# Optimization experiments

Measured on AMD Instinct MI355X. Metric: run time of the kernel, lower is better.

The kernel has to match this reference:

```python
import jax, jax.numpy as jnp
import numpy as np

B, F, D, U = 4096, 32, 64, 256


def setup_inputs() -> dict:
    key = jax.random.key(0)
    k1, k2, k3, k4 = jax.random.split(key, 4)
    embeds = jax.random.normal(k1, (B, F, D), dtype=jnp.float32)
    # glorot-ish scaling for the learned weights
    linear_w = jax.random.normal(k2, (F * D, U), dtype=jnp.float32) * (2.0 / (F * D + U)) ** 0.5
    inner_w = jax.random.normal(k3, (U, F), dtype=jnp.float32) * (2.0 / (U + F)) ** 0.5
    outer_w = jax.random.normal(k4, (U, D, D), dtype=jnp.float32) * (2.0 / (2 * D)) ** 0.5
    return {"embeds": embeds, "linear_w": linear_w, "inner_w": inner_w, "outer_w": outer_w}


def reference(embeds, linear_w, inner_w, outer_w):
    b = embeds.shape[0]
    # linear signal lz: flatten fields and project -> [B, U]
    lz = embeds.reshape(b, -1) @ linear_w
    # inner products: per unit u, delta_u = sum_f w_{u,f} * e_f  -> [B, U, D];
    # lp_inner[b,u] = ||delta_u||^2 (collapses the per-unit TF loop into one einsum)
    delta = jnp.einsum('bfd,uf->bud', embeds, inner_w)
    lp_inner = jnp.sum(jnp.square(delta), axis=2)  # [B, U]
    # outer products: product = fs fs^T with fs = sum_f e_f; lp_outer[b,u] = <product_b, W_u>
    fs = jnp.sum(embeds, axis=1)  # [B, D]
    lp_outer = jnp.einsum('bi,bj,uij->bu', fs, fs, outer_w)  # [B, U]
    return jnp.concatenate([lz, lp_inner, lp_outer], axis=1)  # [B, 3U]
```

## Files before the change

### kernel.cpp

```cpp
#include <hip/hip_runtime.h>
#include <hip/hip_bf16.h>


#define KA 3072
#define KW 7168

typedef __attribute__((ext_vector_type(8))) short short8v;
typedef __attribute__((ext_vector_type(4))) float f32x4;

#define GLOAD(src, dst) __builtin_amdgcn_global_load_lds( \
    (const __attribute__((address_space(1))) void*)(src), \
    (__attribute__((address_space(3))) void*)(dst), 16, 0, 0)

static __device__ __forceinline__ short f2bf(float f) {
    union { float f; unsigned u; } v; v.f = f;
    unsigned r = v.u + 0x7fffu + ((v.u >> 16) & 1u);
    return (short)(r >> 16);
}
static __device__ __forceinline__ float bf2f(short s) {
    union { unsigned u; float f; } v; v.u = ((unsigned)(unsigned short)s) << 16;
    return v.f;
}
static __device__ __forceinline__ int cvtpk(float lo, float hi) {
    int r;
    asm("v_cvt_pk_bf16_f32 %0, %1, %2" : "=v"(r) : "v"(lo), "v"(hi));
    return r;
}

__global__ __launch_bounds__(256) void prep(const float* __restrict__ embeds,
                                            const float* __restrict__ lw,
                                            const float* __restrict__ iw,
                                            const float* __restrict__ ow,
                                            short* __restrict__ A,
                                            short* __restrict__ FST,
                                            short* __restrict__ Wt,
                                            float4* __restrict__ outv) {
    __shared__ float se[2048];
    __shared__ short sebf[2048];
    int t = threadIdx.x;

    if (blockIdx.x >= 4352) {
        size_t i = (size_t)(blockIdx.x - 4352) * 256 + t;
        #pragma unroll
        for (int r = 0; r < 3; ++r)
            outv[i + (size_t)r * 262144] = (float4){0.f, 0.f, 0.f, 0.f};
        return;
    }

    if (blockIdx.x < 4096) {
        int b = blockIdx.x;
        const float* e = embeds + (size_t)b * 2048;
        short* arow = A + (size_t)b * KA;

        float4 v0 = ((const float4*)e)[t * 2];
        float4 v1 = ((const float4*)e)[t * 2 + 1];
        ((float4*)se)[t * 2] = v0;
        ((float4*)se)[t * 2 + 1] = v1;
        short8v sb;
        sb[0] = f2bf(v0.x); sb[1] = f2bf(v0.y); sb[2] = f2bf(v0.z); sb[3] = f2bf(v0.w);
        sb[4] = f2bf(v1.x); sb[5] = f2bf(v1.y); sb[6] = f2bf(v1.z); sb[7] = f2bf(v1.w);
        ((short8v*)sebf)[t] = sb;
        *(short8v*)&arow[t * 8] = sb;

        __syncthreads();
        if (t < 64) {
            float s = 0.f;
            #pragma unroll
            for (int f = 0; f < 32; ++f) s += se[f * 64 + t];
            FST[((size_t)(b >> 7)) * 8192 + t * 128 + (b & 127)] = f2bf(s);
        }

        int wid = t >> 6, lane = t & 63;
        int tm = wid >> 1, tn = wid & 1;
        int lr = lane & 15, lk = (lane >> 4) * 8;
        f32x4 g = {0.f, 0.f, 0.f, 0.f};
        #pragma unroll
        for (int ks = 0; ks < 2; ++ks) {
            short8v a  = *(const short8v*)&sebf[(tm * 16 + lr) * 64 + ks * 32 + lk];
            short8v bb = *(const short8v*)&sebf[(tn * 16 + lr) * 64 + ks * 32 + lk];
            g = __builtin_amdgcn_mfma_f32_16x16x32_bf16(a, bb, g, 0, 0, 0);
        }
        #pragma unroll
        for (int r = 0; r < 4; ++r) {
            int grow = tm * 16 + (lane >> 4) * 4 + r;
            int gcol = tn * 16 + lr;
            arow[2048 + grow * 32 + gcol] = f2bf(g[r]);
        }
    } else {
        int u = blockIdx.x - 4096;
        short* w = Wt + (size_t)u * KW;

        for (int k = t; k < 2048; k += 256) w[k] = f2bf(lw[(size_t)k * 256 + u]);

        if (t < 32) se[t] = iw[u * 32 + t];
        __syncthreads();
        for (int idx = t; idx < 1024; idx += 256)
            w[2048 + idx] = f2bf(se[idx >> 5] * se[idx & 31]);

        const float* owu = ow + (size_t)u * 4096;
        for (int i = t; i < 512; i += 256) {
            float4 a = ((const float4*)owu)[i * 2];
            float4 b = ((const float4*)owu)[i * 2 + 1];
            short8v s;
            s[0] = f2bf(a.x); s[1] = f2bf(a.y); s[2] = f2bf(a.z); s[3] = f2bf(a.w);
            s[4] = f2bf(b.x); s[5] = f2bf(b.y); s[6] = f2bf(b.z); s[7] = f2bf(b.w);
            *(short8v*)&w[3072 + i * 8] = s;
        }
    }
}

__global__ __launch_bounds__(256, 2) void gemm_tile(const short* __restrict__ A,
                                                    const short* __restrict__ Wt,
                                                    const short* __restrict__ FST,
                                                    float* __restrict__ out) {
    __shared__ short As[2][8192];
    __shared__ short Bs[2][8192];

    int id = blockIdx.x;
    int xcd = id & 7, s = id >> 3;
    int mt = xcd * 4 + (s & 3);
    int sc = s >> 2;
    int c = sc & 7, nt = sc >> 3;
    int seg, kc, nk;
    if (c < 2)      { seg = 0; kc = c;     nk = 16; }
    else if (c < 4) { seg = 1; kc = c - 2; nk = 8;  }
    else            { seg = 2; kc = c - 4; nk = 16; }
    int brow = mt * 128, bcol = nt * 128;
    int akoff = (seg == 0) ? kc * 1024 : 2048 + kc * 512;
    int boff  = (seg == 0) ? kc * 1024 : (seg == 1) ? 2048 + kc * 512 : 3072 + kc * 1024;

    int t = threadIdx.x, w = t >> 6, lane = t & 63;
    int wm = w >> 1, wn = w & 1;
    int lr = lane & 15, hi = lane >> 4;
    int srow = t >> 3;
    int soct = (t & 7) ^ (srow & 7);

    const short* Asrc = A  + (size_t)(brow + srow) * KA + akoff + soct * 8;
    const short* Bsrc = Wt + (size_t)(bcol + srow) * KW + boff  + soct * 8;
    const short* Fsrc = FST + (size_t)mt * 8192;

    auto stageA = [&](int p, int kt) {
        #pragma unroll
        for (int i = 0; i < 4; ++i)
            GLOAD(Asrc + (size_t)i * 32 * KA + kt * 64, &As[p][i * 2048 + t * 8]);
    };
    auto stageB = [&](int p, int kt) {
        #pragma unroll
        for (int i = 0; i < 4; ++i)
            GLOAD(Bsrc + (size_t)i * 32 * KW + kt * 64, &Bs[p][i * 2048 + t * 8]);
    };

    f32x4 acc[4][4];
    #pragma unroll
    for (int m = 0; m < 4; ++m)
        #pragma unroll
        for (int n = 0; n < 4; ++n) acc[m][n] = (f32x4){0.f, 0.f, 0.f, 0.f};

    auto compute = [&](const short* a_s, const short* b_s) {
        #pragma unroll
        for (int ks = 0; ks < 2; ++ks) {
            int oct = ((ks * 4 + hi) ^ (lr & 7)) * 8;
            short8v a[4], b[4];
            #pragma unroll
            for (int m = 0; m < 4; ++m)
                a[m] = *(const short8v*)&a_s[(wm * 64 + m * 16 + lr) * 64 + oct];
            #pragma unroll
            for (int n = 0; n < 4; ++n)
                b[n] = *(const short8v*)&b_s[(wn * 64 + n * 16 + lr) * 64 + oct];
            __builtin_amdgcn_s_setprio(1);
            #pragma unroll
            for (int m = 0; m < 4; ++m)
                #pragma unroll
                for (int n = 0; n < 4; ++n)
                    acc[m][n] = __builtin_amdgcn_mfma_f32_16x16x32_bf16(a[m], b[n], acc[m][n], 0, 0, 0);
            __builtin_amdgcn_s_setprio(0);
        }
    };

    if (seg != 2) {
        stageA(0, 0); stageB(0, 0);
        stageA(1, 1); stageB(1, 1);
        __builtin_amdgcn_sched_barrier(0);
        for (int kt = 0; kt < nk; ++kt) {
            int cur = kt & 1;
            if (kt + 1 < nk) asm volatile("s_waitcnt vmcnt(8)" ::: "memory");
            else             asm volatile("s_waitcnt vmcnt(0)" ::: "memory");
            __builtin_amdgcn_s_barrier();
            __builtin_amdgcn_sched_barrier(0);
            compute(As[cur], Bs[cur]);
            __builtin_amdgcn_sched_barrier(0);
            __builtin_amdgcn_s_barrier();
            if (kt + 2 < nk) { stageA(cur, kt + 2); stageB(cur, kt + 2); }
            __builtin_amdgcn_sched_barrier(0);
        }
    } else {
        #pragma unroll
        for (int i = 0; i < 4; ++i)
            GLOAD(Fsrc + i * 2048 + t * 8, &As[0][i * 2048 + t * 8]);
        stageB(0, 0); stageB(1, 1);
        asm volatile("s_waitcnt vmcnt(8)" ::: "memory");
        __builtin_amdgcn_s_barrier();
        __builtin_amdgcn_sched_barrier(0);

        float fj[4][2][8];
        #pragma unroll
        for (int m = 0; m < 4; ++m) {
            int row = wm * 64 + m * 16 + lr;
            #pragma unroll
            for (int ks = 0; ks < 2; ++ks) {
                int j0 = (ks * 4 + hi) * 8;
                #pragma unroll
                for (int e = 0; e < 8; ++e)
                    fj[m][ks][e] = bf2f(As[0][(j0 + e) * 128 + row]);
            }
        }
        for (int kt = 0; kt < nk; ++kt) {
            int cur = kt & 1;
            if (kt + 1 < nk) asm volatile("s_waitcnt vmcnt(4)" ::: "memory");
            else             asm volatile("s_waitcnt vmcnt(0)" ::: "memory");
            __builtin_amdgcn_s_barrier();
            __builtin_amdgcn_sched_barrier(0);
            int iidx = kc * 16 + kt;
            float sv[4];
            #pragma unroll
            for (int m = 0; m < 4; ++m)
                sv[m] = bf2f(As[0][iidx * 128 + wm * 64 + m * 16 + lr]);
            #pragma unroll
            for (int ks = 0; ks < 2; ++ks) {
                int oct = ((ks * 4 + hi) ^ (lr & 7)) * 8;
                short8v b[4];
                #pragma unroll
                for (int n = 0; n < 4; ++n)
                    b[n] = *(const short8v*)&Bs[cur][(wn * 64 + n * 16 + lr) * 64 + oct];
                #pragma unroll
                for (int m = 0; m < 4; ++m) {
                    union { int i32[4]; short8v v; } fa;
                    #pragma unroll
                    for (int q2 = 0; q2 < 4; ++q2)
                        fa.i32[q2] = cvtpk(sv[m] * fj[m][ks][2 * q2], sv[m] * fj[m][ks][2 * q2 + 1]);
                    __builtin_amdgcn_s_setprio(1);
                    #pragma unroll
                    for (int n = 0; n < 4; ++n)
                        acc[m][n] = __builtin_amdgcn_mfma_f32_16x16x32_bf16(fa.v, b[n], acc[m][n], 0, 0, 0);
                    __builtin_amdgcn_s_setprio(0);
                }
            }
            __builtin_amdgcn_sched_barrier(0);
            __builtin_amdgcn_s_barrier();
            if (kt + 2 < nk) stageB(cur, kt + 2);
            __builtin_amdgcn_sched_barrier(0);
        }
    }

    int segbase = seg * 256;
    #pragma unroll
    for (int m = 0; m < 4; ++m) {
        int row0 = brow + wm * 64 + m * 16 + hi * 4;
        #pragma unroll
        for (int n = 0; n < 4; ++n) {
            int col = segbase + bcol + wn * 64 + n * 16 + lr;
            #pragma unroll
            for (int r = 0; r < 4; ++r)
                unsafeAtomicAdd(&out[(size_t)(row0 + r) * 768 + col], acc[m][n][r]);
        }
    }
}

extern "C" void kernel_launch(void* const* d_in, const int* in_sizes, int n_in,
                              void* d_out, int out_size, void* d_ws, size_t ws_size,
                              hipStream_t stream) {
    const float* embeds = (const float*)d_in[0];
    const float* lw = (const float*)d_in[1];
    const float* iw = (const float*)d_in[2];
    const float* ow = (const float*)d_in[3];
    float* out = (float*)d_out;

    short* A   = (short*)d_ws;
    short* Wt  = A + (size_t)4096 * KA;
    short* FST = Wt + (size_t)256 * KW;

    prep<<<dim3(5376), dim3(256), 0, stream>>>(embeds, lw, iw, ow, A, FST, Wt, (float4*)out);
    gemm_tile<<<dim3(512), dim3(256), 0, stream>>>(A, Wt, FST, out);
}
```

Measured before the change: 58.06 us.

## Split-K finer into 896 blocks, drop double buffering for higher occupancy

Every segment now uses 8 K-iterations, with more K chunks for the linear and outer segments, so the grid grows from 512 to 896 blocks. LDS per block is halved by removing the double-buffered async pipeline, and launch bounds ask for 4 blocks per CU. The aim is to fill the GPU better and hide latency through occupancy rather than software pipelining. In exchange, each tile loads synchronously with no overlap inside a block, the priority hints are gone, and more atomic adds go to the output.

```diff
diff --git a/kernel.cpp b/kernel.cpp
--- a/kernel.cpp
+++ b/kernel.cpp
@@ -109,25 +109,26 @@
     }
 }
 
-__global__ __launch_bounds__(256, 2) void gemm_tile(const short* __restrict__ A,
+__global__ __launch_bounds__(256, 4) void gemm_tile(const short* __restrict__ A,
                                                     const short* __restrict__ Wt,
                                                     const short* __restrict__ FST,
                                                     float* __restrict__ out) {
-    __shared__ short As[2][8192];
-    __shared__ short Bs[2][8192];
+    __shared__ short As[8192];
+    __shared__ short Bs[8192];
 
     int id = blockIdx.x;
     int xcd = id & 7, s = id >> 3;
     int mt = xcd * 4 + (s & 3);
-    int sc = s >> 2;
-    int c = sc & 7, nt = sc >> 3;
-    int seg, kc, nk;
-    if (c < 2)      { seg = 0; kc = c;     nk = 16; }
-    else if (c < 4) { seg = 1; kc = c - 2; nk = 8;  }
-    else            { seg = 2; kc = c - 4; nk = 16; }
+    int r5 = s >> 2;
+    int nt = r5 & 1, c = r5 >> 1;
+    int seg, kc;
+    if (c < 4)      { seg = 0; kc = c; }
+    else if (c < 6) { seg = 1; kc = c - 4; }
+    else            { seg = 2; kc = c - 6; }
+    const int nk = 8;
     int brow = mt * 128, bcol = nt * 128;
-    int akoff = (seg == 0) ? kc * 1024 : 2048 + kc * 512;
-    int boff  = (seg == 0) ? kc * 1024 : (seg == 1) ? 2048 + kc * 512 : 3072 + kc * 1024;
+    int akoff = (seg == 0) ? kc * 512 : 2048 + kc * 512;
+    int boff  = (seg == 0) ? kc * 512 : (seg == 1) ? 2048 + kc * 512 : 3072 + kc * 512;
 
     int t = threadIdx.x, w = t >> 6, lane = t & 63;
     int wm = w >> 1, wn = w & 1;
@@ -139,15 +140,15 @@
     const short* Bsrc = Wt + (size_t)(bcol + srow) * KW + boff  + soct * 8;
     const short* Fsrc = FST + (size_t)mt * 8192;
 
-    auto stageA = [&](int p, int kt) {
+    auto stageA = [&](int kt) {
         #pragma unroll
         for (int i = 0; i < 4; ++i)
-            GLOAD(Asrc + (size_t)i * 32 * KA + kt * 64, &As[p][i * 2048 + t * 8]);
+            GLOAD(Asrc + (size_t)i * 32 * KA + kt * 64, &As[i * 2048 + t * 8]);
     };
-    auto stageB = [&](int p, int kt) {
+    auto stageB = [&](int kt) {
         #pragma unroll
         for (int i = 0; i < 4; ++i)
-            GLOAD(Bsrc + (size_t)i * 32 * KW + kt * 64, &Bs[p][i * 2048 + t * 8]);
+            GLOAD(Bsrc + (size_t)i * 32 * KW + kt * 64, &Bs[i * 2048 + t * 8]);
     };
 
     f32x4 acc[4][4];
@@ -156,51 +157,37 @@
         #pragma unroll
         for (int n = 0; n < 4; ++n) acc[m][n] = (f32x4){0.f, 0.f, 0.f, 0.f};
 
-    auto compute = [&](const short* a_s, const short* b_s) {
+    auto compute = [&]() {
         #pragma unroll
         for (int ks = 0; ks < 2; ++ks) {
             int oct = ((ks * 4 + hi) ^ (lr & 7)) * 8;
             short8v a[4], b[4];
             #pragma unroll
             for (int m = 0; m < 4; ++m)
-                a[m] = *(const short8v*)&a_s[(wm * 64 + m * 16 + lr) * 64 + oct];
+                a[m] = *(const short8v*)&As[(wm * 64 + m * 16 + lr) * 64 + oct];
             #pragma unroll
             for (int n = 0; n < 4; ++n)
-                b[n] = *(const short8v*)&b_s[(wn * 64 + n * 16 + lr) * 64 + oct];
-            __builtin_amdgcn_s_setprio(1);
+                b[n] = *(const short8v*)&Bs[(wn * 64 + n * 16 + lr) * 64 + oct];
             #pragma unroll
             for (int m = 0; m < 4; ++m)
                 #pragma unroll
                 for (int n = 0; n < 4; ++n)
                     acc[m][n] = __builtin_amdgcn_mfma_f32_16x16x32_bf16(a[m], b[n], acc[m][n], 0, 0, 0);
-            __builtin_amdgcn_s_setprio(0);
         }
     };
 
     if (seg != 2) {
-        stageA(0, 0); stageB(0, 0);
-        stageA(1, 1); stageB(1, 1);
-        __builtin_amdgcn_sched_barrier(0);
         for (int kt = 0; kt < nk; ++kt) {
-            int cur = kt & 1;
-            if (kt + 1 < nk) asm volatile("s_waitcnt vmcnt(8)" ::: "memory");
-            else             asm volatile("s_waitcnt vmcnt(0)" ::: "memory");
-            __builtin_amdgcn_s_barrier();
-            __builtin_amdgcn_sched_barrier(0);
-            compute(As[cur], Bs[cur]);
-            __builtin_amdgcn_sched_barrier(0);
-            __builtin_amdgcn_s_barrier();
-            if (kt + 2 < nk) { stageA(cur, kt + 2); stageB(cur, kt + 2); }
-            __builtin_amdgcn_sched_barrier(0);
+            stageA(kt); stageB(kt);
+            __syncthreads();
+            compute();
+            __syncthreads();
         }
     } else {
         #pragma unroll
         for (int i = 0; i < 4; ++i)
-            GLOAD(Fsrc + i * 2048 + t * 8, &As[0][i * 2048 + t * 8]);
-        stageB(0, 0); stageB(1, 1);
-        asm volatile("s_waitcnt vmcnt(8)" ::: "memory");
-        __builtin_amdgcn_s_barrier();
-        __builtin_amdgcn_sched_barrier(0);
+            GLOAD(Fsrc + i * 2048 + t * 8, &As[i * 2048 + t * 8]);
+        __syncthreads();
 
         float fj[4][2][8];
         #pragma unroll
@@ -211,44 +198,36 @@
                 int j0 = (ks * 4 + hi) * 8;
                 #pragma unroll
                 for (int e = 0; e < 8; ++e)
-                    fj[m][ks][e] = bf2f(As[0][(j0 + e) * 128 + row]);
+                    fj[m][ks][e] = bf2f(As[(j0 + e) * 128 + row]);
             }
         }
         for (int kt = 0; kt < nk; ++kt) {
-            int cur = kt & 1;
-            if (kt + 1 < nk) asm volatile("s_waitcnt vmcnt(4)" ::: "memory");
-            else             asm volatile("s_waitcnt vmcnt(0)" ::: "memory");
-            __builtin_amdgcn_s_barrier();
-            __builtin_amdgcn_sched_barrier(0);
-            int iidx = kc * 16 + kt;
+            stageB(kt);
+            __syncthreads();
+            int iidx = kc * 8 + kt;
             float sv[4];
             #pragma unroll
             for (int m = 0; m < 4; ++m)
-                sv[m] = bf2f(As[0][iidx * 128 + wm * 64 + m * 16 + lr]);
+                sv[m] = bf2f(As[iidx * 128 + wm * 64 + m * 16 + lr]);
             #pragma unroll
             for (int ks = 0; ks < 2; ++ks) {
                 int oct = ((ks * 4 + hi) ^ (lr & 7)) * 8;
                 short8v b[4];
                 #pragma unroll
                 for (int n = 0; n < 4; ++n)
-                    b[n] = *(const short8v*)&Bs[cur][(wn * 64 + n * 16 + lr) * 64 + oct];
+                    b[n] = *(const short8v*)&Bs[(wn * 64 + n * 16 + lr) * 64 + oct];
                 #pragma unroll
                 for (int m = 0; m < 4; ++m) {
                     union { int i32[4]; short8v v; } fa;
                     #pragma unroll
                     for (int q2 = 0; q2 < 4; ++q2)
                         fa.i32[q2] = cvtpk(sv[m] * fj[m][ks][2 * q2], sv[m] * fj[m][ks][2 * q2 + 1]);
-                    __builtin_amdgcn_s_setprio(1);
                     #pragma unroll
                     for (int n = 0; n < 4; ++n)
                         acc[m][n] = __builtin_amdgcn_mfma_f32_16x16x32_bf16(fa.v, b[n], acc[m][n], 0, 0, 0);
-                    __builtin_amdgcn_s_setprio(0);
                 }
             }
-            __builtin_amdgcn_sched_barrier(0);
-            __builtin_amdgcn_s_barrier();
-            if (kt + 2 < nk) stageB(cur, kt + 2);
-            __builtin_amdgcn_sched_barrier(0);
+            __syncthreads();
         }
     }
 
@@ -280,5 +259,5 @@
     short* FST = Wt + (size_t)256 * KW;
 
     prep<<<dim3(5376), dim3(256), 0, stream>>>(embeds, lw, iw, ow, A, FST, Wt, (float4*)out);
-    gemm_tile<<<dim3(512), dim3(256), 0, stream>>>(A, Wt, FST, out);
-}
+    gemm_tile<<<dim3(896), dim3(256), 0, stream>>>(A, Wt, FST, out);
+}
```

Measured after the change: 90.70 us. 56.2% more time.

## Exploit symmetry of Gram and outer products with packed upper-triangle features

Applied to the files above, without the earlier changes.

Both quadratic terms are symmetric forms, so the inner-product Gram matrix (32x32) and the fs*fs^T outer product (64x64) are packed as lower triangles. The matching weights are folded accordingly: off-diagonal terms are doubled for the inner weights, and W+W^T is formed for the outer weights. This shrinks the K dimension from 7168 to 4736 and replaces the special on-the-fly outer-product path with the uniform pipelined GEMM loop. The seg 1 tile now writes its output directly instead of using atomics, and only the other columns are zeroed. The trade-off is more prep work per row: triangular index math with sqrt and materialising 2080 outer-product elements per batch row, plus bf16 rounding of fs_i*fs_j products.

```diff
diff --git a/kernel.cpp b/kernel.cpp
--- a/kernel.cpp
+++ b/kernel.cpp
@@ -2,8 +2,7 @@
 #include <hip/hip_bf16.h>
 
 
-#define KA 3072
-#define KW 7168
+#define KA2 4736
 
 typedef __attribute__((ext_vector_type(8))) short short8v;
 typedef __attribute__((ext_vector_type(4))) float f32x4;
@@ -17,14 +16,11 @@
     unsigned r = v.u + 0x7fffu + ((v.u >> 16) & 1u);
     return (short)(r >> 16);
 }
-static __device__ __forceinline__ float bf2f(short s) {
-    union { unsigned u; float f; } v; v.u = ((unsigned)(unsigned short)s) << 16;
-    return v.f;
-}
-static __device__ __forceinline__ int cvtpk(float lo, float hi) {
-    int r;
-    asm("v_cvt_pk_bf16_f32 %0, %1, %2" : "=v"(r) : "v"(lo), "v"(hi));
-    return r;
+static __device__ __forceinline__ void tri_ij(int idx, int& i, int& j) {
+    i = (int)((sqrtf(8.f * (float)idx + 1.f) - 1.f) * 0.5f);
+    while ((i + 1) * (i + 2) / 2 <= idx) ++i;
+    while (i * (i + 1) / 2 > idx) --i;
+    j = idx - i * (i + 1) / 2;
 }
 
 __global__ __launch_bounds__(256) void prep(const float* __restrict__ embeds,
@@ -32,25 +28,25 @@
                                             const float* __restrict__ iw,
                                             const float* __restrict__ ow,
                                             short* __restrict__ A,
-                                            short* __restrict__ FST,
                                             short* __restrict__ Wt,
                                             float4* __restrict__ outv) {
     __shared__ float se[2048];
     __shared__ short sebf[2048];
+    __shared__ float fsm[64];
     int t = threadIdx.x;
 
     if (blockIdx.x >= 4352) {
-        size_t i = (size_t)(blockIdx.x - 4352) * 256 + t;
-        #pragma unroll
-        for (int r = 0; r < 3; ++r)
-            outv[i + (size_t)r * 262144] = (float4){0.f, 0.f, 0.f, 0.f};
+        int idx = (blockIdx.x - 4352) * 256 + t;
+        int row = idx >> 7, c128 = idx & 127;
+        int f4col = c128 + (c128 >= 64 ? 64 : 0);
+        outv[(size_t)row * 192 + f4col] = (float4){0.f, 0.f, 0.f, 0.f};
         return;
     }
 
     if (blockIdx.x < 4096) {
         int b = blockIdx.x;
         const float* e = embeds + (size_t)b * 2048;
-        short* arow = A + (size_t)b * KA;
+        short* arow = A + (size_t)b * KA2;
 
         float4 v0 = ((const float4*)e)[t * 2];
         float4 v1 = ((const float4*)e)[t * 2 + 1];
@@ -67,7 +63,7 @@
             float s = 0.f;
             #pragma unroll
             for (int f = 0; f < 32; ++f) s += se[f * 64 + t];
-            FST[((size_t)(b >> 7)) * 8192 + t * 128 + (b & 127)] = f2bf(s);
+            fsm[t] = s;
         }
 
         int wid = t >> 6, lane = t & 63;
@@ -84,34 +80,44 @@
         for (int r = 0; r < 4; ++r) {
             int grow = tm * 16 + (lane >> 4) * 4 + r;
             int gcol = tn * 16 + lr;
-            arow[2048 + grow * 32 + gcol] = f2bf(g[r]);
-        }
+            if (gcol <= grow)
+                arow[2048 + grow * (grow + 1) / 2 + gcol] = f2bf(g[r]);
+        }
+        if (t < 48) arow[2048 + 528 + t] = 0;
+
+        __syncthreads();
+        for (int idx = t; idx < 2080; idx += 256) {
+            int i, j; tri_ij(idx, i, j);
+            arow[2624 + idx] = f2bf(fsm[i] * fsm[j]);
+        }
+        if (t < 32) arow[2624 + 2080 + t] = 0;
     } else {
         int u = blockIdx.x - 4096;
-        short* w = Wt + (size_t)u * KW;
+        short* w = Wt + (size_t)u * KA2;
 
         for (int k = t; k < 2048; k += 256) w[k] = f2bf(lw[(size_t)k * 256 + u]);
 
         if (t < 32) se[t] = iw[u * 32 + t];
         __syncthreads();
-        for (int idx = t; idx < 1024; idx += 256)
-            w[2048 + idx] = f2bf(se[idx >> 5] * se[idx & 31]);
+        for (int idx = t; idx < 528; idx += 256) {
+            int i, j; tri_ij(idx, i, j);
+            float v = se[i] * se[j];
+            w[2048 + idx] = f2bf(i == j ? v : 2.f * v);
+        }
+        if (t < 48) w[2048 + 528 + t] = 0;
 
         const float* owu = ow + (size_t)u * 4096;
-        for (int i = t; i < 512; i += 256) {
-            float4 a = ((const float4*)owu)[i * 2];
-            float4 b = ((const float4*)owu)[i * 2 + 1];
-            short8v s;
-            s[0] = f2bf(a.x); s[1] = f2bf(a.y); s[2] = f2bf(a.z); s[3] = f2bf(a.w);
-            s[4] = f2bf(b.x); s[5] = f2bf(b.y); s[6] = f2bf(b.z); s[7] = f2bf(b.w);
-            *(short8v*)&w[3072 + i * 8] = s;
-        }
+        for (int idx = t; idx < 2080; idx += 256) {
+            int i, j; tri_ij(idx, i, j);
+            float v = (i == j) ? owu[i * 65] : (owu[i * 64 + j] + owu[j * 64 + i]);
+            w[2624 + idx] = f2bf(v);
+        }
+        if (t < 32) w[2624 + 2080 + t] = 0;
     }
 }
 
 __global__ __launch_bounds__(256, 2) void gemm_tile(const short* __restrict__ A,
                                                     const short* __restrict__ Wt,
-                                                    const short* __restrict__ FST,
                                                     float* __restrict__ out) {
     __shared__ short As[2][8192];
     __shared__ short Bs[2][8192];
@@ -119,15 +125,13 @@
     int id = blockIdx.x;
     int xcd = id & 7, s = id >> 3;
     int mt = xcd * 4 + (s & 3);
-    int sc = s >> 2;
-    int c = sc & 7, nt = sc >> 3;
-    int seg, kc, nk;
-    if (c < 2)      { seg = 0; kc = c;     nk = 16; }
-    else if (c < 4) { seg = 1; kc = c - 2; nk = 8;  }
-    else            { seg = 2; kc = c - 4; nk = 16; }
+    int q = s >> 2;
+    int nt = q & 1, c = q >> 1;
+    int seg, nk, koff;
+    if (c < 4)       { seg = 0; nk = 8;  koff = c * 512; }
+    else if (c == 4) { seg = 1; nk = 9;  koff = 2048; }
+    else             { seg = 2; nk = 11; koff = 2624 + (c - 5) * 704; }
     int brow = mt * 128, bcol = nt * 128;
-    int akoff = (seg == 0) ? kc * 1024 : 2048 + kc * 512;
-    int boff  = (seg == 0) ? kc * 1024 : (seg == 1) ? 2048 + kc * 512 : 3072 + kc * 1024;
 
     int t = threadIdx.x, w = t >> 6, lane = t & 63;
     int wm = w >> 1, wn = w & 1;
@@ -135,19 +139,18 @@
     int srow = t >> 3;
     int soct = (t & 7) ^ (srow & 7);
 
-    const short* Asrc = A  + (size_t)(brow + srow) * KA + akoff + soct * 8;
-    const short* Bsrc = Wt + (size_t)(bcol + srow) * KW + boff  + soct * 8;
-    const short* Fsrc = FST + (size_t)mt * 8192;
+    const short* Asrc = A  + (size_t)(brow + srow) * KA2 + koff + soct * 8;
+    const short* Bsrc = Wt + (size_t)(bcol + srow) * KA2 + koff + soct * 8;
 
     auto stageA = [&](int p, int kt) {
         #pragma unroll
         for (int i = 0; i < 4; ++i)
-            GLOAD(Asrc + (size_t)i * 32 * KA + kt * 64, &As[p][i * 2048 + t * 8]);
+            GLOAD(Asrc + (size_t)i * 32 * KA2 + kt * 64, &As[p][i * 2048 + t * 8]);
     };
     auto stageB = [&](int p, int kt) {
         #pragma unroll
         for (int i = 0; i < 4; ++i)
-            GLOAD(Bsrc + (size_t)i * 32 * KW + kt * 64, &Bs[p][i * 2048 + t * 8]);
+            GLOAD(Bsrc + (size_t)i * 32 * KA2 + kt * 64, &Bs[p][i * 2048 + t * 8]);
     };
 
     f32x4 acc[4][4];
@@ -177,91 +180,46 @@
         }
     };
 
-    if (seg != 2) {
-        stageA(0, 0); stageB(0, 0);
-        stageA(1, 1); stageB(1, 1);
-        __builtin_amdgcn_sched_barrier(0);
-        for (int kt = 0; kt < nk; ++kt) {
-            int cur = kt & 1;
-            if (kt + 1 < nk) asm volatile("s_waitcnt vmcnt(8)" ::: "memory");
-            else             asm volatile("s_waitcnt vmcnt(0)" ::: "memory");
-            __builtin_amdgcn_s_barrier();
-            __builtin_amdgcn_sched_barrier(0);
-            compute(As[cur], Bs[cur]);
-            __builtin_amdgcn_sched_barrier(0);
-            __builtin_amdgcn_s_barrier();
-            if (kt + 2 < nk) { stageA(cur, kt + 2); stageB(cur, kt + 2); }
-            __builtin_amdgcn_sched_barrier(0);
-        }
-    } else {
-        #pragma unroll
-        for (int i = 0; i < 4; ++i)
-            GLOAD(Fsrc + i * 2048 + t * 8, &As[0][i * 2048 + t * 8]);
-        stageB(0, 0); stageB(1, 1);
-        asm volatile("s_waitcnt vmcnt(8)" ::: "memory");
+    stageA(0, 0); stageB(0, 0);
+    stageA(1, 1); stageB(1, 1);
+    __builtin_amdgcn_sched_barrier(0);
+    for (int kt = 0; kt < nk; ++kt) {
+        int cur = kt & 1;
+        if (kt + 1 < nk) asm volatile("s_waitcnt vmcnt(8)" ::: "memory");
+        else             asm volatile("s_waitcnt vmcnt(0)" ::: "memory");
         __builtin_amdgcn_s_barrier();
         __builtin_amdgcn_sched_barrier(0);
-
-        float fj[4][2][8];
+        compute(As[cur], Bs[cur]);
+        __builtin_amdgcn_sched_barrier(0);
+        __builtin_amdgcn_s_barrier();
+        if (kt + 2 < nk) { stageA(cur, kt + 2); stageB(cur, kt + 2); }
+        __builtin_amdgcn_sched_barrier(0);
+    }
+
+    int segbase = seg * 256;
+    if (seg == 1) {
         #pragma unroll
         for (int m = 0; m < 4; ++m) {
-            int row = wm * 64 + m * 16 + lr;
-            #pragma unroll
-            for (int ks = 0; ks < 2; ++ks) {
-                int j0 = (ks * 4 + hi) * 8;
+            int row0 = brow + wm * 64 + m * 16 + hi * 4;
+            #pragma unroll
+            for (int n = 0; n < 4; ++n) {
+                int col = segbase + bcol + wn * 64 + n * 16 + lr;
                 #pragma unroll
-                for (int e = 0; e < 8; ++e)
-                    fj[m][ks][e] = bf2f(As[0][(j0 + e) * 128 + row]);
+                for (int r = 0; r < 4; ++r)
+                    out[(size_t)(row0 + r) * 768 + col] = acc[m][n][r];
             }
         }
-        for (int kt = 0; kt < nk; ++kt) {
-            int cur = kt & 1;
-            if (kt + 1 < nk) asm volatile("s_waitcnt vmcnt(4)" ::: "memory");
-            else             asm volatile("s_waitcnt vmcnt(0)" ::: "memory");
-            __builtin_amdgcn_s_barrier();
-            __builtin_amdgcn_sched_barrier(0);
-            int iidx = kc * 16 + kt;
-            float sv[4];
-            #pragma unroll
-            for (int m = 0; m < 4; ++m)
-                sv[m] = bf2f(As[0][iidx * 128 + wm * 64 + m * 16 + lr]);
-            #pragma unroll
-            for (int ks = 0; ks < 2; ++ks) {
-                int oct = ((ks * 4 + hi) ^ (lr & 7)) * 8;
-                short8v b[4];
+    } else {
+        #pragma unroll
+        for (int m = 0; m < 4; ++m) {
+            int row0 = brow + wm * 64 + m * 16 + hi * 4;
+            #pragma unroll
+            for (int n = 0; n < 4; ++n) {
+                int col = segbase + bcol + wn * 64 + n * 16 + lr;
                 #pragma unroll
-                for (int n = 0; n < 4; ++n)
-                    b[n] = *(const short8v*)&Bs[cur][(wn * 64 + n * 16 + lr) * 64 + oct];
-                #pragma unroll
-                for (int m = 0; m < 4; ++m) {
-                    union { int i32[4]; short8v v; } fa;
-                    #pragma unroll
-                    for (int q2 = 0; q2 < 4; ++q2)
-                        fa.i32[q2] = cvtpk(sv[m] * fj[m][ks][2 * q2], sv[m] * fj[m][ks][2 * q2 + 1]);
-                    __builtin_amdgcn_s_setprio(1);
-                    #pragma unroll
-                    for (int n = 0; n < 4; ++n)
-                        acc[m][n] = __builtin_amdgcn_mfma_f32_16x16x32_bf16(fa.v, b[n], acc[m][n], 0, 0, 0);
-                    __builtin_amdgcn_s_setprio(0);
-                }
+                for (int r = 0; r < 4; ++r)
+                    unsafeAtomicAdd(&out[(size_t)(row0 + r) * 768 + col], acc[m][n][r]);
             }
-            __builtin_amdgcn_sched_barrier(0);
-            __builtin_amdgcn_s_barrier();
-            if (kt + 2 < nk) stageB(cur, kt + 2);
-            __builtin_amdgcn_sched_barrier(0);
-        }
-    }
-
-    int segbase = seg * 256;
-    #pragma unroll
-    for (int m = 0; m < 4; ++m) {
-        int row0 = brow + wm * 64 + m * 16 + hi * 4;
-        #pragma unroll
-        for (int n = 0; n < 4; ++n) {
-            int col = segbase + bcol + wn * 64 + n * 16 + lr;
-            #pragma unroll
-            for (int r = 0; r < 4; ++r)
-                unsafeAtomicAdd(&out[(size_t)(row0 + r) * 768 + col], acc[m][n][r]);
         }
     }
 }
@@ -275,10 +233,9 @@
     const float* ow = (const float*)d_in[3];
     float* out = (float*)d_out;
 
-    short* A   = (short*)d_ws;
-    short* Wt  = A + (size_t)4096 * KA;
-    short* FST = Wt + (size_t)256 * KW;
-
-    prep<<<dim3(5376), dim3(256), 0, stream>>>(embeds, lw, iw, ow, A, FST, Wt, (float4*)out);
-    gemm_tile<<<dim3(512), dim3(256), 0, stream>>>(A, Wt, FST, out);
-}
+    short* A  = (short*)d_ws;
+    short* Wt = A + (size_t)4096 * KA2;
+
+    prep<<<dim3(6400), dim3(256), 0, stream>>>(embeds, lw, iw, ow, A, Wt, (float4*)out);
+    gemm_tile<<<dim3(512), dim3(256), 0, stream>>>(A, Wt, out);
+}
```

Measured after the change: 64.84 us. 11.7% more time.
